# Kernel tuning notes

Hardware: AMD Instinct MI355X
Metric: run time of the kernel (lower is better)

## Reference

```python
import jax, jax.numpy as jnp
import numpy as np

# Quantum circuit closed form: per wire i, state |0> -> RX(x_i) -> RY(theta_i),
# then <PauliZ_i> = cos(theta_i) * cos(x_i). No entangling gates, so wires are
# independent and the whole per-token loop collapses to one elementwise op.

B, S, E = 8, 4096, 512
NQ, FFN = 8, 2048

def setup_inputs() -> dict:
    key = jax.random.key(0)
    ks = jax.random.split(key, 6)
    return {
        "x": jax.random.normal(ks[0], (B, S, E), dtype=jnp.float32),
        "theta": jax.random.normal(ks[1], (NQ,), dtype=jnp.float32),
        "W1": jax.random.normal(ks[2], (FFN, NQ), dtype=jnp.float32) * (1.0 / np.sqrt(NQ)),
        "b1": jax.random.normal(ks[3], (FFN,), dtype=jnp.float32) * 0.01,
        "W2": jax.random.normal(ks[4], (E, FFN), dtype=jnp.float32) * (1.0 / np.sqrt(FFN)),
        "b2": jax.random.normal(ks[5], (E,), dtype=jnp.float32) * 0.01,
    }

def reference(x, theta, W1, b1, W2, b2):
    n_qubits = theta.shape[0]
    # token_slice = x[:, :, :n_qubits]; <Z> = cos(theta) * cos(x)
    q_out = jnp.cos(x[..., :n_qubits]) * jnp.cos(theta)        # [B, S, NQ]
    h = jax.nn.relu(jnp.einsum('bsq,fq->bsf', q_out, W1) + b1)  # [B, S, FFN]
    out = jnp.einsum('bsf,ef->bse', h, W2) + b2                 # [B, S, E]
    return out
```

## Files before the change

kernel.cpp:

```cpp
#include <hip/hip_runtime.h>
#include <math.h>

typedef __attribute__((ext_vector_type(8)))  short short8;
typedef __attribute__((ext_vector_type(16))) float float16_t;

__device__ __forceinline__ short f2bf(float f) {
    union { float f; unsigned u; } c; c.f = f;
    unsigned u = c.u + 0x7fffu + ((c.u >> 16) & 1u);
    return (short)(u >> 16);
}
__device__ __forceinline__ unsigned fbits(float f) {
    union { float f; unsigned u; } c; c.f = f; return c.u;
}
__device__ __forceinline__ float16_t zero16() {
    float16_t z;
#pragma unroll
    for (int r = 0; r < 16; ++r) z[r] = 0.0f;
    return z;
}

__global__ __launch_bounds__(256) void prep_kernel(
    const float* __restrict__ x, const float* __restrict__ theta,
    const float* __restrict__ W1, const float* __restrict__ b1,
    const float* __restrict__ W2,
    short* __restrict__ W2P, short* __restrict__ Qz, short* __restrict__ W1z)
{
    int gid = blockIdx.x * 256 + threadIdx.x;
    if (gid < 131072) {
        int lane = gid & 63;
        int ks   = (gid >> 6) & 127;
        int nt   = gid >> 13;
        int n = nt * 32 + (lane & 31);
        int k = ks * 16 + (lane >> 5) * 8;
        const float4* p = (const float4*)(W2 + n * 2048 + k);
        float4 v0 = p[0], v1 = p[1];
        short8 o;
        o[0] = f2bf(v0.x); o[1] = f2bf(v0.y); o[2] = f2bf(v0.z); o[3] = f2bf(v0.w);
        o[4] = f2bf(v1.x); o[5] = f2bf(v1.y); o[6] = f2bf(v1.z); o[7] = f2bf(v1.w);
        *(short8*)(W2P + gid * 8) = o;
    } else if (gid < 131072 + 32768) {
        int t = gid - 131072;
        const float4* xp = (const float4*)(x + t * 512);
        float4 x0 = xp[0], x1 = xp[1];
        float xv[8] = {x0.x, x0.y, x0.z, x0.w, x1.x, x1.y, x1.z, x1.w};
        short8 q;
#pragma unroll
        for (int c = 0; c < 8; ++c)
            q[c] = f2bf(cosf(xv[c]) * cosf(theta[c]));
        *(short8*)(Qz + t * 8) = q;
    } else if (gid < 131072 + 32768 + 2048) {
        int f = gid - (131072 + 32768);
        const float4* wp = (const float4*)(W1 + f * 8);
        float4 w0 = wp[0], w1 = wp[1];
        short8 wv;
        wv[0] = f2bf(w0.x); wv[1] = f2bf(w0.y); wv[2] = f2bf(w0.z); wv[3] = f2bf(w0.w);
        wv[4] = f2bf(w1.x); wv[5] = f2bf(w1.y); wv[6] = f2bf(w1.z); wv[7] = f2bf(w1.w);
        short8 bz = {0,0,0,0,0,0,0,0};
        bz[0] = f2bf(b1[f]);
        *(short8*)(W1z + f * 16) = wv;
        *(short8*)(W1z + f * 16 + 8) = bz;
    }
}

__device__ __forceinline__ void stage1_tile(
    short8 a1, const short8* qf, short* __restrict__ dst,
    int wx, int wy, int lh, int l31)
{
#pragma unroll
    for (int i = 0; i < 2; ++i) {
        float16_t d1 = __builtin_amdgcn_mfma_f32_32x32x16_bf16(
            a1, qf[i], zero16(), 0, 0, 0);
        const int m = wy * 64 + i * 32 + l31;
#pragma unroll
        for (int g = 0; g < 4; ++g) {
            float v0 = fmaxf(d1[g * 4 + 0], 0.0f);
            float v1 = fmaxf(d1[g * 4 + 1], 0.0f);
            float v2 = fmaxf(d1[g * 4 + 2], 0.0f);
            float v3 = fmaxf(d1[g * 4 + 3], 0.0f);
            uint2 pp;
            pp.x = __builtin_amdgcn_perm(fbits(v1), fbits(v0), 0x07060302u);
            pp.y = __builtin_amdgcn_perm(fbits(v3), fbits(v2), 0x07060302u);
            *(uint2*)(dst + (wx * 4 + g) * 1024 + m * 8 + 4 * lh) = pp;
        }
    }
}

__global__ __launch_bounds__(256, 2) void ffn_kernel(
    const short* __restrict__ Qz, const short* __restrict__ W1z,
    const short* __restrict__ W2P, const float* __restrict__ b2,
    float* __restrict__ out)
{
    __shared__ short Hs[2 * 8192];

    const int tid  = threadIdx.x;
    const int lane = tid & 63;
    const int w    = tid >> 6;
    const int wy = w & 1, wx = w >> 1;
    const int l31 = lane & 31, lh = lane >> 5;
    const int bid = blockIdx.x;
    const int nt = bid & 1, mt = bid >> 1;
    const int m0 = mt * 128, n0 = nt * 256;

    short8 qf[2];
#pragma unroll
    for (int i = 0; i < 2; ++i) {
        short8 v = {0,0,0,0,0,0,0,0};
        if (lh == 0)
            v = *(const short8*)(Qz + (m0 + wy * 64 + i * 32 + l31) * 8);
        else
            v[0] = (short)0x3F80;
        qf[i] = v;
    }

    int w2base[4];
#pragma unroll
    for (int j = 0; j < 4; ++j)
        w2base[j] = (nt * 8 + wx * 4 + j) * 65536 + lane * 8;

    float16_t acc[2][4];
#pragma unroll
    for (int i = 0; i < 2; ++i)
#pragma unroll
        for (int j = 0; j < 4; ++j) acc[i][j] = zero16();

    {
        short8 a1 = *(const short8*)(W1z + (wx * 32 + l31) * 16 + lh * 8);
        stage1_tile(a1, qf, Hs, wx, wy, lh, l31);
    }
    __syncthreads();

    for (int kt = 0; kt < 32; ++kt) {
        const int p = kt & 1;

        short8 a1 = {0,0,0,0,0,0,0,0};
        if (kt < 31)
            a1 = *(const short8*)(W1z + ((kt + 1) * 64 + wx * 32 + l31) * 16 + lh * 8);

        short8 bfv[4][4];
#pragma unroll
        for (int ks = 0; ks < 4; ++ks)
#pragma unroll
            for (int j = 0; j < 4; ++j)
                bfv[ks][j] = *(const short8*)(W2P + w2base[j] + (kt * 4 + ks) * 512);

        if (kt < 31)
            stage1_tile(a1, qf, Hs + (p ^ 1) * 8192, wx, wy, lh, l31);

        const short* rd = Hs + p * 8192;
#pragma unroll
        for (int ks = 0; ks < 4; ++ks) {
            short8 af[2];
#pragma unroll
            for (int i = 0; i < 2; ++i)
                af[i] = *(const short8*)(rd + (ks * 2 + lh) * 1024 +
                                         (wy * 64 + i * 32 + l31) * 8);
#pragma unroll
            for (int i = 0; i < 2; ++i)
#pragma unroll
                for (int j = 0; j < 4; ++j)
                    acc[i][j] = __builtin_amdgcn_mfma_f32_32x32x16_bf16(
                        af[i], bfv[ks][j], acc[i][j], 0, 0, 0);
        }
        __syncthreads();
    }

#pragma unroll
    for (int j = 0; j < 4; ++j) {
        const int n = n0 + wx * 128 + j * 32 + l31;
        const float b2v = b2[n];
#pragma unroll
        for (int i = 0; i < 2; ++i) {
            const int base = (m0 + wy * 64 + i * 32 + 4 * lh) * 512 + n;
#pragma unroll
            for (int r = 0; r < 16; ++r) {
                const int off = ((r & 3) + 8 * (r >> 2)) * 512;
                out[base + off] = acc[i][j][r] + b2v;
            }
        }
    }
}

extern "C" void kernel_launch(void* const* d_in, const int* in_sizes, int n_in,
                              void* d_out, int out_size, void* d_ws, size_t ws_size,
                              hipStream_t stream)
{
    const float* x     = (const float*)d_in[0];
    const float* theta = (const float*)d_in[1];
    const float* W1    = (const float*)d_in[2];
    const float* b1    = (const float*)d_in[3];
    const float* W2    = (const float*)d_in[4];
    const float* b2    = (const float*)d_in[5];
    float* out = (float*)d_out;

    short* W2P = (short*)d_ws;
    short* Qz  = (short*)((char*)d_ws + 2097152);
    short* W1z = (short*)((char*)d_ws + 2621440);

    prep_kernel<<<648, 256, 0, stream>>>(x, theta, W1, b1, W2, W2P, Qz, W1z);
    ffn_kernel<<<512, 256, 0, stream>>>(Qz, W1z, W2P, b2, out);
}
```

Measured before the change: 173.8 us.

## Software-pipeline W2 and W1 register loads across k-iterations in FFN kernel

Splits each k-tile's W2 fragment loads into two halves (A/B) and prefetches the first half of the next iteration while the second half's MFMAs run. The W1 fragment for stage 1 is likewise loaded one iteration ahead. This aims to hide global-memory latency behind MFMA work instead of stalling at the top of each iteration. In exchange it raises register pressure, which with launch bounds (256,2) could cause spills.

New measurement: 172.0 us. Within noise of the previous version (-1.0%).

```diff
diff --git a/kernel.cpp b/kernel.cpp
--- a/kernel.cpp
+++ b/kernel.cpp
@@ -112,10 +112,11 @@
         qf[i] = v;
     }
 
-    int w2base[4];
+    int w2off[4];
 #pragma unroll
     for (int j = 0; j < 4; ++j)
-        w2base[j] = (nt * 8 + wx * 4 + j) * 65536 + lane * 8;
+        w2off[j] = (nt * 8 + wx * 4 + j) * 65536 + lane * 8;
+    const int a1off = (wx * 32 + l31) * 16 + lh * 8;
 
     float16_t acc[2][4];
 #pragma unroll
@@ -123,32 +124,41 @@
 #pragma unroll
         for (int j = 0; j < 4; ++j) acc[i][j] = zero16();
 
+    const short* W2Pk = W2P;
+    const short* W1za = W1z + 2048;
+
+    short8 bfvA[2][4], bfvB[2][4];
+#pragma unroll
+    for (int ks = 0; ks < 2; ++ks)
+#pragma unroll
+        for (int j = 0; j < 4; ++j)
+            bfvA[ks][j] = *(const short8*)(W2Pk + w2off[j] + ks * 512);
+    short8 a1n = *(const short8*)(W1z + 1024 + a1off);
     {
-        short8 a1 = *(const short8*)(W1z + (wx * 32 + l31) * 16 + lh * 8);
-        stage1_tile(a1, qf, Hs, wx, wy, lh, l31);
+        short8 a1_0 = *(const short8*)(W1z + a1off);
+        stage1_tile(a1_0, qf, Hs, wx, wy, lh, l31);
     }
     __syncthreads();
 
     for (int kt = 0; kt < 32; ++kt) {
         const int p = kt & 1;
-
-        short8 a1 = {0,0,0,0,0,0,0,0};
+        short* wr = Hs + (p ^ 1) * 8192;
+        const short* rd = Hs + p * 8192;
+
+#pragma unroll
+        for (int ks = 0; ks < 2; ++ks)
+#pragma unroll
+            for (int j = 0; j < 4; ++j)
+                bfvB[ks][j] = *(const short8*)(W2Pk + w2off[j] + (ks + 2) * 512);
+
         if (kt < 31)
-            a1 = *(const short8*)(W1z + ((kt + 1) * 64 + wx * 32 + l31) * 16 + lh * 8);
-
-        short8 bfv[4][4];
-#pragma unroll
-        for (int ks = 0; ks < 4; ++ks)
-#pragma unroll
-            for (int j = 0; j < 4; ++j)
-                bfv[ks][j] = *(const short8*)(W2P + w2base[j] + (kt * 4 + ks) * 512);
-
-        if (kt < 31)
-            stage1_tile(a1, qf, Hs + (p ^ 1) * 8192, wx, wy, lh, l31);
-
-        const short* rd = Hs + p * 8192;
-#pragma unroll
-        for (int ks = 0; ks < 4; ++ks) {
+            stage1_tile(a1n, qf, wr, wx, wy, lh, l31);
+        if (kt < 30)
+            a1n = *(const short8*)(W1za + a1off);
+        W1za += 1024;
+
+#pragma unroll
+        for (int ks = 0; ks < 2; ++ks) {
             short8 af[2];
 #pragma unroll
             for (int i = 0; i < 2; ++i)
@@ -159,8 +169,33 @@
 #pragma unroll
                 for (int j = 0; j < 4; ++j)
                     acc[i][j] = __builtin_amdgcn_mfma_f32_32x32x16_bf16(
-                        af[i], bfv[ks][j], acc[i][j], 0, 0, 0);
-        }
+                        af[i], bfvA[ks][j], acc[i][j], 0, 0, 0);
+        }
+
+        W2Pk += 2048;
+        if (kt < 31) {
+#pragma unroll
+            for (int ks = 0; ks < 2; ++ks)
+#pragma unroll
+                for (int j = 0; j < 4; ++j)
+                    bfvA[ks][j] = *(const short8*)(W2Pk + w2off[j] + ks * 512);
+        }
+
+#pragma unroll
+        for (int ks = 0; ks < 2; ++ks) {
+            short8 af[2];
+#pragma unroll
+            for (int i = 0; i < 2; ++i)
+                af[i] = *(const short8*)(rd + ((ks + 2) * 2 + lh) * 1024 +
+                                         (wy * 64 + i * 32 + l31) * 8);
+#pragma unroll
+            for (int i = 0; i < 2; ++i)
+#pragma unroll
+                for (int j = 0; j < 4; ++j)
+                    acc[i][j] = __builtin_amdgcn_mfma_f32_32x32x16_bf16(
+                        af[i], bfvB[ks][j], acc[i][j], 0, 0, 0);
+        }
+
         __syncthreads();
     }
 
```
